# Kernel optimization log

Measured on AMD Instinct MI355X. Metric: run time of the kernel, lower is better.

## Reference

```python
import jax, jax.numpy as jnp
import numpy as np

B, C, L = 2, 512, 4096
HEADS, KV_HEADS, DIM_HEAD = 8, 2, 64
ROTARY_DIM = 32  # int(64 * 0.5), even
ROPE_THETA = 10000.0
SCALE = DIM_HEAD ** -0.5


def _rotate_half(x):
    # pairs (x0, x1) -> (-x1, x0), interleaved layout
    x = x.reshape(*x.shape[:-1], x.shape[-1] // 2, 2)
    x1, x2 = x[..., 0], x[..., 1]
    return jnp.stack([-x2, x1], axis=-1).reshape(*x.shape[:-2], x.shape[-2] * 2)


def _rope_sin_cos(seq_len, rotary_dim, theta, dtype):
    positions = jnp.arange(seq_len, dtype=dtype)
    half = rotary_dim // 2
    inv_freq = theta ** (-2.0 * jnp.arange(half, dtype=dtype) / rotary_dim)
    sinusoid = positions[:, None] * inv_freq[None, :]          # (L, half)
    sin = jnp.repeat(jnp.sin(sinusoid), 2, axis=-1)            # (L, rotary_dim) interleaved
    cos = jnp.repeat(jnp.cos(sinusoid), 2, axis=-1)
    return sin[None, None], cos[None, None]                    # (1,1,L,rotary_dim)


def setup_inputs() -> dict:
    key = jax.random.key(0)
    kx, kq, kkv, ko = jax.random.split(key, 4)
    s = 0.02
    return {
        "x": jax.random.normal(kx, (B, C, L), dtype=jnp.float32),
        "Wq": jax.random.normal(kq, (HEADS * DIM_HEAD, C), dtype=jnp.float32) * s,
        "Wkv": jax.random.normal(kkv, (2 * KV_HEADS * DIM_HEAD, C), dtype=jnp.float32) * s,
        "Wo": jax.random.normal(ko, (C, HEADS * DIM_HEAD), dtype=jnp.float32) * s,
    }


def reference(x, Wq, Wkv, Wo):
    b, c, l = x.shape
    x_t = jnp.swapaxes(x, 1, 2)                                 # (B, L, C)
    q = x_t @ Wq.T                                              # (B, L, H*dh)
    kv = x_t @ Wkv.T                                            # (B, L, KVH*2*dh)
    q = q.reshape(b, l, HEADS, DIM_HEAD).transpose(0, 2, 1, 3)  # (B, H, L, dh)
    kv = kv.reshape(b, l, KV_HEADS, 2 * DIM_HEAD).transpose(0, 2, 1, 3)
    k, v = jnp.split(kv, 2, axis=-1)                            # (B, KVH, L, dh) each

    sin, cos = _rope_sin_cos(l, ROTARY_DIM, ROPE_THETA, x.dtype)
    q_rot, q_pass = q[..., :ROTARY_DIM], q[..., ROTARY_DIM:]
    k_rot, k_pass = k[..., :ROTARY_DIM], k[..., ROTARY_DIM:]
    q_rot = q_rot * cos + _rotate_half(q_rot) * sin
    k_rot = k_rot * cos + _rotate_half(k_rot) * sin
    q = jnp.concatenate([q_rot, q_pass], axis=-1)
    k = jnp.concatenate([k_rot, k_pass], axis=-1)

    rep = HEADS // KV_HEADS
    k = jnp.repeat(k, rep, axis=1)                              # (B, H, L, dh)
    v = jnp.repeat(v, rep, axis=1)

    q = q * SCALE
    attn = jnp.einsum('bhid,bhjd->bhij', q, k)                  # (B, H, L, L)
    attn = jax.nn.softmax(attn, axis=-1)
    out = jnp.einsum('bhij,bhjd->bhid', attn, v)                # (B, H, L, dh)
    out = out.transpose(0, 2, 1, 3).reshape(b, l, HEADS * DIM_HEAD)
    out = out @ Wo.T                                            # (B, L, C)
    return jnp.swapaxes(out, 1, 2)                              # (B, C, L)
```

## Files before the change

kernel.cpp:

```cpp
#include <hip/hip_runtime.h>

using f16   = _Float16;
using f16x2 = __attribute__((ext_vector_type(2))) f16;
using f16x4 = __attribute__((ext_vector_type(4))) f16;
using f16x8 = __attribute__((ext_vector_type(8))) f16;
using f32x4 = __attribute__((ext_vector_type(4))) float;

#define L_ 4096
#define C_ 512

static __device__ __forceinline__ float fast_exp2(float x) {
#if __has_builtin(__builtin_amdgcn_exp2f)
  return __builtin_amdgcn_exp2f(x);
#else
  float r; asm("v_exp_f32 %0, %1" : "=v"(r) : "v"(x)); return r;
#endif
}

static __device__ __forceinline__ f16x2 pk2(float a, float b) {
  return __builtin_bit_cast(f16x2, __builtin_amdgcn_cvt_pkrtz(a, b));
}

#define WS_SC    0u
#define WS_WQKV  524288u
#define WS_WO    1310720u
#define WS_Q     1835008u
#define WS_K     10223616u
#define WS_VT    12320768u
#define WS_ATT   14417920u
#define WS_OP    22806528u
#define WS_LS2   56360960u
#define WS_END2  56885248u

__global__ __launch_bounds__(256) void prep_kernel(
    const float* __restrict__ Wq, const float* __restrict__ Wkv,
    const float* __restrict__ Wo,
    f16* __restrict__ wqkv, f16* __restrict__ wo16, float2* __restrict__ sc) {
  int t = blockIdx.x * 256 + threadIdx.x;
  if (t < 98304) {
    int idx = t * 4;
    float4 v = (idx < 262144) ? *(const float4*)(Wq + idx)
                              : *(const float4*)(Wkv + (idx - 262144));
    f16x4 o = {(f16)v.x, (f16)v.y, (f16)v.z, (f16)v.w};
    *(f16x4*)(wqkv + idx) = o;
  } else if (t < 163840) {
    int idx = (t - 98304) * 4;
    float4 v = *(const float4*)(Wo + idx);
    f16x4 o = {(f16)v.x, (f16)v.y, (f16)v.z, (f16)v.w};
    *(f16x4*)(wo16 + idx) = o;
  } else if (t < 229376) {
    int e = t - 163840;
    int l = e >> 4, p = e & 15;
    float invf = exp2f(-(float)p * (13.287712379549449f / 16.0f));
    float ang = (float)l * invf;
    sc[e] = make_float2(sinf(ang), cosf(ang));
  }
}

__global__ __launch_bounds__(256) void qkv_kernel(
    const float* __restrict__ x, const f16* __restrict__ wqkv,
    const float2* __restrict__ sc,
    f16* __restrict__ Qo, f16* __restrict__ Ko, f16* __restrict__ Vto) {
  int bid = blockIdx.x;
  int b   = bid / 384;
  int rem = bid % 384;
  int ot  = rem >> 7;
  int lt  = rem & 127;
  int wave = threadIdx.x >> 6, lane = threadIdx.x & 63;
  int lo = lane & 15, hi = lane >> 4;
  int obase = ot * 256 + wave * 64;
  int lbase = lt * 32;
  const float* xb = x + (size_t)b * C_ * L_;

  f32x4 acc[4][2] = {};
  for (int kc = 0; kc < 512; kc += 32) {
    f16x8 aw[4];
#pragma unroll
    for (int oc = 0; oc < 4; ++oc)
      aw[oc] = *(const f16x8*)(wqkv + (obase + oc * 16 + lo) * 512 + kc + hi * 8);
#pragma unroll
    for (int lc = 0; lc < 2; ++lc) {
      f16x8 bx;
#pragma unroll
      for (int i = 0; i < 8; ++i)
        bx[i] = (f16)xb[(size_t)(kc + hi * 8 + i) * L_ + lbase + lc * 16 + lo];
#pragma unroll
      for (int oc = 0; oc < 4; ++oc)
        acc[oc][lc] = __builtin_amdgcn_mfma_f32_16x16x32_f16(aw[oc], bx, acc[oc][lc], 0, 0, 0);
    }
  }

  bool is_q = obase < 512;
  int  og   = obase - 512;
  int  kvh  = is_q ? 0 : (og >> 7);
  bool is_v = (!is_q) && ((og & 127) == 64);
  int  h    = obase >> 6;
  const float QSCALE = 0.125f * 1.44269504088896340736f;

#pragma unroll
  for (int oc = 0; oc < 4; ++oc) {
#pragma unroll
    for (int lc = 0; lc < 2; ++lc) {
      f32x4 v = acc[oc][lc];
      int l = lbase + lc * 16 + lo;
      int d = oc * 16 + hi * 4;
      if (!is_v && oc < 2) {
        int p0 = d >> 1;
        float2 s0 = sc[l * 16 + p0];
        float2 s1 = sc[l * 16 + p0 + 1];
        float a0 = v[0], a1 = v[1], a2 = v[2], a3 = v[3];
        v[0] = a0 * s0.y - a1 * s0.x;
        v[1] = a1 * s0.y + a0 * s0.x;
        v[2] = a2 * s1.y - a3 * s1.x;
        v[3] = a3 * s1.y + a2 * s1.x;
      }
      if (is_q) {
        f16x4 st = {(f16)(v[0] * QSCALE), (f16)(v[1] * QSCALE),
                    (f16)(v[2] * QSCALE), (f16)(v[3] * QSCALE)};
        *(f16x4*)(Qo + (((size_t)b * 8 + h) * L_ + l) * 64 + d) = st;
      } else if (!is_v) {
        f16x4 st = {(f16)v[0], (f16)v[1], (f16)v[2], (f16)v[3]};
        *(f16x4*)(Ko + (((size_t)b * 2 + kvh) * L_ + l) * 64 + d) = st;
      } else {
#pragma unroll
        for (int i = 0; i < 4; ++i)
          Vto[(((size_t)b * 2 + kvh) * 64 + d + i) * L_ + l] = (f16)v[i];
      }
    }
  }
}

template <int SPLIT>
__global__ __launch_bounds__(512) void attn_kernel(
    const f16* __restrict__ Qi, const f16* __restrict__ Ki,
    const f16* __restrict__ Vti, f16* __restrict__ att,
    f16* __restrict__ opart, float* __restrict__ lsews) {
  __shared__ __align__(16) char smem[2][16384];
  int bid  = blockIdx.x;
  int half = (SPLIT > 1) ? (bid >> 7) : 0;
  int rem7 = bid & 127;
  int b   = rem7 >> 6;
  int rr  = rem7 & 63;
  int h   = rr >> 3;
  int qt  = rr & 7;
  int tid  = threadIdx.x;
  int wave = tid >> 6, lane = tid & 63;
  int lo = lane & 15, hi = lane >> 4;
  int kvh = h >> 2;
  const f16*  Qp   = Qi + ((size_t)(b * 8 + h) * L_) * 64;
  const char* Ksrc = (const char*)(Ki  + ((size_t)(b * 2 + kvh)) * L_ * 64)
                     + (size_t)half * (L_ / SPLIT) * 128;
  const char* Vsrc = (const char*)(Vti + ((size_t)(b * 2 + kvh)) * 64 * L_)
                     + (size_t)half * (L_ / SPLIT) * 2;

  int lqb = qt * 512 + wave * 64;
  f16x8 qf[4][2];
#pragma unroll
  for (int qi = 0; qi < 4; ++qi)
#pragma unroll
    for (int hf = 0; hf < 2; ++hf)
      qf[qi][hf] = *(const f16x8*)(Qp + (size_t)(lqb + qi * 16 + lo) * 64 + hf * 32 + hi * 8);

  int c0 = tid;
  int r0 = c0 >> 3, m0 = c0 & 7;
  int cb0 = m0 << 4;
  int dstK0 = r0 * 128 + (cb0 ^ ((r0 & 7) << 4));
  int ca0 = (m0 >> 2) * 64 + ((2 * m0) & 3) * 16 + ((m0 >> 1) & 1) * 8;
  int dstV0a = r0 * 128 + (ca0 ^ ((r0 & 7) << 4));
  int dstV0b = r0 * 128 + ((ca0 + 16) ^ ((r0 & 7) << 4));

  f16x8 sK0, sV0;
#define STAGE_LOAD(t) do {                                            \
    sK0 = *(const f16x8*)(Ksrc + (size_t)(t) * 8192 + c0 * 16);       \
    sV0 = *(const f16x8*)(Vsrc + (size_t)r0 * 8192 + (t) * 128 + cb0);\
  } while (0)
#define STAGE_WRITE(base_) do {                                       \
    char* kb_ = (char*)(base_);                                       \
    *(f16x8*)(kb_ + dstK0) = sK0;                                     \
    *(f16x4*)(kb_ + 8192 + dstV0a) = __builtin_shufflevector(sV0, sV0, 0, 1, 2, 3); \
    *(f16x4*)(kb_ + 8192 + dstV0b) = __builtin_shufflevector(sV0, sV0, 4, 5, 6, 7); \
  } while (0)

  f32x4 oacc[4][4] = {};
  f32x4 lse[4] = {};
  const f16x8 ones8 = {(f16)1.f, (f16)1.f, (f16)1.f, (f16)1.f,
                       (f16)1.f, (f16)1.f, (f16)1.f, (f16)1.f};
  int swz = (lo & 7) << 4;

#define COMPUTE(buf_) do {                                                          \
    const char* kb = (const char*)(buf_);                                           \
    const char* vb = kb + 8192;                                                     \
    _Pragma("unroll")                                                               \
    for (int jp = 0; jp < 2; ++jp) {                                                \
      f32x4 s[2][4] = {};                                                           \
      __builtin_amdgcn_s_setprio(1);                                                \
      _Pragma("unroll")                                                             \
      for (int jj = 0; jj < 2; ++jj) {                                              \
        int j = jp * 2 + jj;                                                        \
        f16x8 ka0 = *(const f16x8*)(kb + (j * 16 + lo) * 128 + ((hi * 16) ^ swz));  \
        f16x8 ka1 = *(const f16x8*)(kb + (j * 16 + lo) * 128 + ((64 + hi * 16) ^ swz)); \
        _Pragma("unroll")                                                           \
        for (int qi = 0; qi < 4; ++qi) {                                            \
          s[jj][qi] = __builtin_amdgcn_mfma_f32_16x16x32_f16(ka0, qf[qi][0], s[jj][qi], 0, 0, 0); \
          s[jj][qi] = __builtin_amdgcn_mfma_f32_16x16x32_f16(ka1, qf[qi][1], s[jj][qi], 0, 0, 0); \
        }                                                                           \
      }                                                                             \
      __builtin_amdgcn_s_setprio(0);                                                \
      f16x8 pc[4];                                                                  \
      _Pragma("unroll")                                                             \
      for (int qi = 0; qi < 4; ++qi) {                                              \
        f16x2 a0 = pk2(fast_exp2(s[0][qi][0]), fast_exp2(s[0][qi][1]));             \
        f16x2 a1 = pk2(fast_exp2(s[0][qi][2]), fast_exp2(s[0][qi][3]));             \
        f16x2 b0 = pk2(fast_exp2(s[1][qi][0]), fast_exp2(s[1][qi][1]));             \
        f16x2 b1 = pk2(fast_exp2(s[1][qi][2]), fast_exp2(s[1][qi][3]));             \
        f16x4 l4 = __builtin_shufflevector(a0, a1, 0, 1, 2, 3);                     \
        f16x4 h4 = __builtin_shufflevector(b0, b1, 0, 1, 2, 3);                     \
        pc[qi] = __builtin_shufflevector(l4, h4, 0, 1, 2, 3, 4, 5, 6, 7);           \
      }                                                                             \
      __builtin_amdgcn_s_setprio(1);                                                \
      _Pragma("unroll")                                                             \
      for (int dc = 0; dc < 4; ++dc) {                                              \
        f16x8 vv = *(const f16x8*)(vb + (dc * 16 + lo) * 128 + ((jp * 64 + hi * 16) ^ swz)); \
        _Pragma("unroll")                                                           \
        for (int qi = 0; qi < 4; ++qi)                                              \
          oacc[dc][qi] = __builtin_amdgcn_mfma_f32_16x16x32_f16(vv, pc[qi], oacc[dc][qi], 0, 0, 0); \
      }                                                                             \
      _Pragma("unroll")                                                             \
      for (int qi = 0; qi < 4; ++qi)                                                \
        lse[qi] = __builtin_amdgcn_mfma_f32_16x16x32_f16(ones8, pc[qi], lse[qi], 0, 0, 0); \
      __builtin_amdgcn_s_setprio(0);                                                \
    }                                                                               \
  } while (0)

  const int NT = 64 / SPLIT;
  STAGE_LOAD(0);
  STAGE_WRITE(smem[0]);
  __syncthreads();

  for (int t = 0; t < NT; t += 2) {
    STAGE_LOAD(t + 1);
    COMPUTE(smem[0]);
    STAGE_WRITE(smem[1]);
    __syncthreads();
    if (t + 2 < NT) STAGE_LOAD(t + 2);
    COMPUTE(smem[1]);
    if (t + 2 < NT) STAGE_WRITE(smem[0]);
    __syncthreads();
  }

#pragma unroll
  for (int qi = 0; qi < 4; ++qi) {
    int lq = lqb + qi * 16 + lo;
    if constexpr (SPLIT > 1) {
      size_t obase = (((size_t)(half * 2 + b) * 8 + h) * L_ + lq) * 64;
#pragma unroll
      for (int dc = 0; dc < 4; ++dc) {
        f16x4 st;
#pragma unroll
        for (int i = 0; i < 4; ++i) st[i] = (f16)oacc[dc][qi][i];
        *(f16x4*)(opart + obase + dc * 16 + hi * 4) = st;
      }
      if (hi == 0)
        lsews[((size_t)(half * 2 + b) * 8 + h) * L_ + lq] = lse[qi][0];
    } else {
      float inv = 1.f / lse[qi][0];
#pragma unroll
      for (int dc = 0; dc < 4; ++dc) {
        f16x4 st;
#pragma unroll
        for (int i = 0; i < 4; ++i) st[i] = (f16)(oacc[dc][qi][i] * inv);
        *(f16x4*)(att + ((size_t)b * L_ + lq) * 512 + h * 64 + dc * 16 + hi * 4) = st;
      }
    }
  }
#undef STAGE_LOAD
#undef STAGE_WRITE
#undef COMPUTE
}

template <int SPLIT>
__global__ __launch_bounds__(256) void combine_kernel(
    const f16* __restrict__ opart, const float* __restrict__ lsews,
    f16* __restrict__ att) {
  int t = blockIdx.x * 256 + threadIdx.x;
  int d4 = t & 15;
  int lq = (t >> 4) & 4095;
  int h  = (t >> 16) & 7;
  int b  = t >> 19;
  const size_t HS  = (size_t)2 * 8 * 4096 * 64;
  const size_t LSS = (size_t)2 * 8 * 4096;
  size_t base  = (((size_t)b * 8 + h) * 4096 + lq) * 64 + d4 * 4;
  size_t lbase = ((size_t)b * 8 + h) * 4096 + lq;
  float o[4] = {};
  float ls = 0.f;
#pragma unroll
  for (int s = 0; s < SPLIT; ++s) {
    f16x4 op = *(const f16x4*)(opart + s * HS + base);
#pragma unroll
    for (int i = 0; i < 4; ++i) o[i] += (float)op[i];
    ls += lsews[s * LSS + lbase];
  }
  float inv = 1.f / ls;
  f16x4 st;
#pragma unroll
  for (int i = 0; i < 4; ++i) st[i] = (f16)(o[i] * inv);
  *(f16x4*)(att + ((size_t)b * 4096 + lq) * 512 + h * 64 + d4 * 4) = st;
}

__global__ __launch_bounds__(256) void oproj_kernel(
    const f16* __restrict__ att, const f16* __restrict__ wo16,
    float* __restrict__ out) {
  int bid = blockIdx.x;
  int b   = bid / 256;
  int rem = bid % 256;
  int ct  = rem >> 7;
  int lt  = rem & 127;
  int wave = threadIdx.x >> 6, lane = threadIdx.x & 63;
  int lo = lane & 15, hi = lane >> 4;
  int cobase = ct * 256 + wave * 64;
  int lbase  = lt * 32;
  const f16* ab = att + (size_t)b * L_ * 512;

  f32x4 acc[4][2] = {};
  for (int kc = 0; kc < 512; kc += 32) {
    f16x8 aw[4];
#pragma unroll
    for (int cc = 0; cc < 4; ++cc)
      aw[cc] = *(const f16x8*)(wo16 + (cobase + cc * 16 + lo) * 512 + kc + hi * 8);
#pragma unroll
    for (int lc = 0; lc < 2; ++lc) {
      f16x8 bx = *(const f16x8*)(ab + (size_t)(lbase + lc * 16 + lo) * 512 + kc + hi * 8);
#pragma unroll
      for (int cc = 0; cc < 4; ++cc)
        acc[cc][lc] = __builtin_amdgcn_mfma_f32_16x16x32_f16(aw[cc], bx, acc[cc][lc], 0, 0, 0);
    }
  }
  float* ob = out + (size_t)b * C_ * L_;
#pragma unroll
  for (int cc = 0; cc < 4; ++cc)
#pragma unroll
    for (int lc = 0; lc < 2; ++lc) {
      int l = lbase + lc * 16 + lo;
#pragma unroll
      for (int i = 0; i < 4; ++i) {
        int co = cobase + cc * 16 + hi * 4 + i;
        ob[(size_t)co * L_ + l] = acc[cc][lc][i];
      }
    }
}

extern "C" void kernel_launch(void* const* d_in, const int* in_sizes, int n_in,
                              void* d_out, int out_size, void* d_ws, size_t ws_size,
                              hipStream_t stream) {
  const float* x   = (const float*)d_in[0];
  const float* Wq  = (const float*)d_in[1];
  const float* Wkv = (const float*)d_in[2];
  const float* Wo  = (const float*)d_in[3];
  char* ws = (char*)d_ws;
  float2* sc  = (float2*)(ws + WS_SC);
  f16* wqkv   = (f16*)(ws + WS_WQKV);
  f16* wo16   = (f16*)(ws + WS_WO);
  f16* Qb     = (f16*)(ws + WS_Q);
  f16* Kb     = (f16*)(ws + WS_K);
  f16* Vtb    = (f16*)(ws + WS_VT);
  f16* attb   = (f16*)(ws + WS_ATT);
  f16* opb    = (f16*)(ws + WS_OP);
  float* lsb  = (float*)(ws + WS_LS2);

  prep_kernel<<<1024, 256, 0, stream>>>(Wq, Wkv, Wo, wqkv, wo16, sc);
  qkv_kernel<<<768, 256, 0, stream>>>(x, wqkv, sc, Qb, Kb, Vtb);
  if (ws_size >= (size_t)WS_END2) {
    attn_kernel<2><<<256, 512, 0, stream>>>(Qb, Kb, Vtb, attb, opb, lsb);
    combine_kernel<2><<<4096, 256, 0, stream>>>(opb, lsb, attb);
  } else {
    attn_kernel<1><<<128, 512, 0, stream>>>(Qb, Kb, Vtb, attb, opb, lsb);
  }
  oproj_kernel<<<512, 256, 0, stream>>>(attb, wo16, (float*)d_out);
}
```

Measured before the change: 144.5 us.

## Fuse split-KV combine into output projection and halve attention block size

The attention kernel now launches 256-thread blocks covering 256 query rows each, with each thread staging two K/V chunks per tile. The launch doubles the grid to 512 blocks for better CU coverage and occupancy. The separate combine kernel is removed. The output projection reads both partial outputs and their log-sum-exp sums directly, normalizes them while building the MFMA B operand, and so avoids writing and re-reading the intermediate attention buffer. In exchange, the projection does redundant combine work per column tile (two ct tiles) and reads partials with strided 64-element accesses.

```diff
diff --git a/kernel.cpp b/kernel.cpp
--- a/kernel.cpp
+++ b/kernel.cpp
@@ -131,18 +131,18 @@
 }
 
 template <int SPLIT>
-__global__ __launch_bounds__(512) void attn_kernel(
+__global__ __launch_bounds__(256) void attn_kernel(
     const f16* __restrict__ Qi, const f16* __restrict__ Ki,
     const f16* __restrict__ Vti, f16* __restrict__ att,
     f16* __restrict__ opart, float* __restrict__ lsews) {
   __shared__ __align__(16) char smem[2][16384];
   int bid  = blockIdx.x;
-  int half = (SPLIT > 1) ? (bid >> 7) : 0;
-  int rem7 = bid & 127;
-  int b   = rem7 >> 6;
-  int rr  = rem7 & 63;
-  int h   = rr >> 3;
-  int qt  = rr & 7;
+  int half = (SPLIT > 1) ? (bid >> 8) : 0;
+  int rem8 = bid & 255;
+  int b   = rem8 >> 7;
+  int rr  = rem8 & 127;
+  int h   = rr >> 4;
+  int qt  = rr & 15;
   int tid  = threadIdx.x;
   int wave = tid >> 6, lane = tid & 63;
   int lo = lane & 15, hi = lane >> 4;
@@ -153,7 +153,7 @@
   const char* Vsrc = (const char*)(Vti + ((size_t)(b * 2 + kvh)) * 64 * L_)
                      + (size_t)half * (L_ / SPLIT) * 2;
 
-  int lqb = qt * 512 + wave * 64;
+  int lqb = qt * 256 + wave * 64;
   f16x8 qf[4][2];
 #pragma unroll
   for (int qi = 0; qi < 4; ++qi)
@@ -161,24 +161,34 @@
     for (int hf = 0; hf < 2; ++hf)
       qf[qi][hf] = *(const f16x8*)(Qp + (size_t)(lqb + qi * 16 + lo) * 64 + hf * 32 + hi * 8);
 
-  int c0 = tid;
+  int c0 = tid, c1 = tid + 256;
   int r0 = c0 >> 3, m0 = c0 & 7;
-  int cb0 = m0 << 4;
+  int r1 = c1 >> 3, m1 = c1 & 7;
+  int cb0 = m0 << 4, cb1 = m1 << 4;
   int dstK0 = r0 * 128 + (cb0 ^ ((r0 & 7) << 4));
+  int dstK1 = r1 * 128 + (cb1 ^ ((r1 & 7) << 4));
   int ca0 = (m0 >> 2) * 64 + ((2 * m0) & 3) * 16 + ((m0 >> 1) & 1) * 8;
+  int ca1 = (m1 >> 2) * 64 + ((2 * m1) & 3) * 16 + ((m1 >> 1) & 1) * 8;
   int dstV0a = r0 * 128 + (ca0 ^ ((r0 & 7) << 4));
   int dstV0b = r0 * 128 + ((ca0 + 16) ^ ((r0 & 7) << 4));
-
-  f16x8 sK0, sV0;
+  int dstV1a = r1 * 128 + (ca1 ^ ((r1 & 7) << 4));
+  int dstV1b = r1 * 128 + ((ca1 + 16) ^ ((r1 & 7) << 4));
+
+  f16x8 sK0, sK1, sV0, sV1;
 #define STAGE_LOAD(t) do {                                            \
     sK0 = *(const f16x8*)(Ksrc + (size_t)(t) * 8192 + c0 * 16);       \
+    sK1 = *(const f16x8*)(Ksrc + (size_t)(t) * 8192 + c1 * 16);       \
     sV0 = *(const f16x8*)(Vsrc + (size_t)r0 * 8192 + (t) * 128 + cb0);\
+    sV1 = *(const f16x8*)(Vsrc + (size_t)r1 * 8192 + (t) * 128 + cb1);\
   } while (0)
 #define STAGE_WRITE(base_) do {                                       \
     char* kb_ = (char*)(base_);                                       \
     *(f16x8*)(kb_ + dstK0) = sK0;                                     \
+    *(f16x8*)(kb_ + dstK1) = sK1;                                     \
     *(f16x4*)(kb_ + 8192 + dstV0a) = __builtin_shufflevector(sV0, sV0, 0, 1, 2, 3); \
     *(f16x4*)(kb_ + 8192 + dstV0b) = __builtin_shufflevector(sV0, sV0, 4, 5, 6, 7); \
+    *(f16x4*)(kb_ + 8192 + dstV1a) = __builtin_shufflevector(sV1, sV1, 0, 1, 2, 3); \
+    *(f16x4*)(kb_ + 8192 + dstV1b) = __builtin_shufflevector(sV1, sV1, 4, 5, 6, 7); \
   } while (0)
 
   f32x4 oacc[4][4] = {};
@@ -278,33 +288,68 @@
 #undef COMPUTE
 }
 
-template <int SPLIT>
-__global__ __launch_bounds__(256) void combine_kernel(
+__global__ __launch_bounds__(256) void oproj_fused_kernel(
     const f16* __restrict__ opart, const float* __restrict__ lsews,
-    f16* __restrict__ att) {
-  int t = blockIdx.x * 256 + threadIdx.x;
-  int d4 = t & 15;
-  int lq = (t >> 4) & 4095;
-  int h  = (t >> 16) & 7;
-  int b  = t >> 19;
+    const f16* __restrict__ wo16, float* __restrict__ out) {
+  int bid = blockIdx.x;
+  int b   = bid / 256;
+  int rem = bid % 256;
+  int ct  = rem >> 7;
+  int lt  = rem & 127;
+  int wave = threadIdx.x >> 6, lane = threadIdx.x & 63;
+  int lo = lane & 15, hi = lane >> 4;
+  int cobase = ct * 256 + wave * 64;
+  int lbase  = lt * 32;
   const size_t HS  = (size_t)2 * 8 * 4096 * 64;
   const size_t LSS = (size_t)2 * 8 * 4096;
-  size_t base  = (((size_t)b * 8 + h) * 4096 + lq) * 64 + d4 * 4;
-  size_t lbase = ((size_t)b * 8 + h) * 4096 + lq;
-  float o[4] = {};
-  float ls = 0.f;
-#pragma unroll
-  for (int s = 0; s < SPLIT; ++s) {
-    f16x4 op = *(const f16x4*)(opart + s * HS + base);
-#pragma unroll
-    for (int i = 0; i < 4; ++i) o[i] += (float)op[i];
-    ls += lsews[s * LSS + lbase];
-  }
-  float inv = 1.f / ls;
-  f16x4 st;
-#pragma unroll
-  for (int i = 0; i < 4; ++i) st[i] = (f16)(o[i] * inv);
-  *(f16x4*)(att + ((size_t)b * 4096 + lq) * 512 + h * 64 + d4 * 4) = st;
+
+  float inv[2][8];
+#pragma unroll
+  for (int lc = 0; lc < 2; ++lc) {
+    int l = lbase + lc * 16 + lo;
+#pragma unroll
+    for (int h = 0; h < 8; ++h) {
+      size_t lidx = ((size_t)b * 8 + h) * L_ + l;
+      inv[lc][h] = 1.f / (lsews[lidx] + lsews[LSS + lidx]);
+    }
+  }
+
+  f32x4 acc[4][2] = {};
+  for (int kc = 0; kc < 512; kc += 32) {
+    f16x8 aw[4];
+#pragma unroll
+    for (int cc = 0; cc < 4; ++cc)
+      aw[cc] = *(const f16x8*)(wo16 + (cobase + cc * 16 + lo) * 512 + kc + hi * 8);
+#pragma unroll
+    for (int lc = 0; lc < 2; ++lc) {
+      int l = lbase + lc * 16 + lo;
+      int o = kc + hi * 8;
+      int h = o >> 6, d = o & 63;
+      size_t base = (((size_t)b * 8 + h) * L_ + l) * 64 + d;
+      f16x8 p0 = *(const f16x8*)(opart + base);
+      f16x8 p1 = *(const f16x8*)(opart + HS + base);
+      float iv = inv[lc][h];
+      f16x8 bx;
+#pragma unroll
+      for (int i = 0; i < 8; ++i)
+        bx[i] = (f16)(((float)p0[i] + (float)p1[i]) * iv);
+#pragma unroll
+      for (int cc = 0; cc < 4; ++cc)
+        acc[cc][lc] = __builtin_amdgcn_mfma_f32_16x16x32_f16(aw[cc], bx, acc[cc][lc], 0, 0, 0);
+    }
+  }
+  float* ob = out + (size_t)b * C_ * L_;
+#pragma unroll
+  for (int cc = 0; cc < 4; ++cc)
+#pragma unroll
+    for (int lc = 0; lc < 2; ++lc) {
+      int l = lbase + lc * 16 + lo;
+#pragma unroll
+      for (int i = 0; i < 4; ++i) {
+        int co = cobase + cc * 16 + hi * 4 + i;
+        ob[(size_t)co * L_ + l] = acc[cc][lc][i];
+      }
+    }
 }
 
 __global__ __launch_bounds__(256) void oproj_kernel(
@@ -370,10 +415,10 @@
   prep_kernel<<<1024, 256, 0, stream>>>(Wq, Wkv, Wo, wqkv, wo16, sc);
   qkv_kernel<<<768, 256, 0, stream>>>(x, wqkv, sc, Qb, Kb, Vtb);
   if (ws_size >= (size_t)WS_END2) {
-    attn_kernel<2><<<256, 512, 0, stream>>>(Qb, Kb, Vtb, attb, opb, lsb);
-    combine_kernel<2><<<4096, 256, 0, stream>>>(opb, lsb, attb);
+    attn_kernel<2><<<512, 256, 0, stream>>>(Qb, Kb, Vtb, attb, opb, lsb);
+    oproj_fused_kernel<<<512, 256, 0, stream>>>(opb, lsb, wo16, (float*)d_out);
   } else {
-    attn_kernel<1><<<128, 512, 0, stream>>>(Qb, Kb, Vtb, attb, opb, lsb);
-  }
-  oproj_kernel<<<512, 256, 0, stream>>>(attb, wo16, (float*)d_out);
-}
+    attn_kernel<1><<<256, 256, 0, stream>>>(Qb, Kb, Vtb, attb, opb, lsb);
+    oproj_kernel<<<512, 256, 0, stream>>>(attb, wo16, (float*)d_out);
+  }
+}
```

Measured after the change: 158.0 us. 9.3% more time.

## Pre-swizzle K/V tiles in projection and load them straight into LDS

Applied to the files above, without the earlier changes.

The projection kernel now writes K and V to global memory already tiled and XOR-swizzled in exactly the shared-memory layout the attention kernel uses. The attention kernel can then copy each tile with 16-byte global_load_lds transfers directly into LDS, skipping the round trip through registers and the separate LDS writes. The double-buffered loop becomes one stage per iteration with a single barrier. In exchange, the layouts of the two kernels are now tightly coupled, and correctness relies on the barrier waiting for the async LDS loads to finish.

```diff
diff --git a/kernel.cpp b/kernel.cpp
--- a/kernel.cpp
+++ b/kernel.cpp
@@ -19,6 +19,12 @@
 
 static __device__ __forceinline__ f16x2 pk2(float a, float b) {
   return __builtin_bit_cast(f16x2, __builtin_amdgcn_cvt_pkrtz(a, b));
+}
+
+static __device__ __forceinline__ void gl16(const char* g, char* l) {
+  __builtin_amdgcn_global_load_lds(
+      (const __attribute__((address_space(1))) unsigned int*)g,
+      (__attribute__((address_space(3))) unsigned int*)l, 16, 0, 0);
 }
 
 #define WS_SC    0u
@@ -120,11 +126,22 @@
         *(f16x4*)(Qo + (((size_t)b * 8 + h) * L_ + l) * 64 + d) = st;
       } else if (!is_v) {
         f16x4 st = {(f16)v[0], (f16)v[1], (f16)v[2], (f16)v[3]};
-        *(f16x4*)(Ko + (((size_t)b * 2 + kvh) * L_ + l) * 64 + d) = st;
+        int t = l >> 6, r = l & 63;
+        int u = (d >> 3) ^ (r & 7);
+        int w = (hi & 1) * 8;
+        char* Kb = (char*)Ko + (size_t)(b * 2 + kvh) * (L_ * 128);
+        *(f16x4*)(Kb + (size_t)t * 8192 + r * 128 + u * 16 + w) = st;
       } else {
-#pragma unroll
-        for (int i = 0; i < 4; ++i)
-          Vto[(((size_t)b * 2 + kvh) * 64 + d + i) * L_ + l] = (f16)v[i];
+        int t = l >> 6, kk = l & 63;
+        int m = kk >> 3, i8 = kk & 7;
+        int ca = (m >> 2) * 64 + ((2 * m) & 3) * 16 + ((m >> 1) & 1) * 8;
+        int bcol = ca + (i8 < 4 ? 2 * i8 : 8 + 2 * i8);
+        char* Vb = (char*)Vto + (size_t)(b * 2 + kvh) * (L_ * 128);
+#pragma unroll
+        for (int i = 0; i < 4; ++i) {
+          int rv = d + i;
+          *(f16*)(Vb + (size_t)t * 8192 + rv * 128 + (bcol ^ ((rv & 7) << 4))) = (f16)v[i];
+        }
       }
     }
   }
@@ -148,10 +165,10 @@
   int lo = lane & 15, hi = lane >> 4;
   int kvh = h >> 2;
   const f16*  Qp   = Qi + ((size_t)(b * 8 + h) * L_) * 64;
-  const char* Ksrc = (const char*)(Ki  + ((size_t)(b * 2 + kvh)) * L_ * 64)
+  const char* Ksrc = (const char*)Ki  + (size_t)(b * 2 + kvh) * (L_ * 128)
                      + (size_t)half * (L_ / SPLIT) * 128;
-  const char* Vsrc = (const char*)(Vti + ((size_t)(b * 2 + kvh)) * 64 * L_)
-                     + (size_t)half * (L_ / SPLIT) * 2;
+  const char* Vsrc = (const char*)Vti + (size_t)(b * 2 + kvh) * (L_ * 128)
+                     + (size_t)half * (L_ / SPLIT) * 128;
 
   int lqb = qt * 512 + wave * 64;
   f16x8 qf[4][2];
@@ -162,23 +179,9 @@
       qf[qi][hf] = *(const f16x8*)(Qp + (size_t)(lqb + qi * 16 + lo) * 64 + hf * 32 + hi * 8);
 
   int c0 = tid;
-  int r0 = c0 >> 3, m0 = c0 & 7;
-  int cb0 = m0 << 4;
-  int dstK0 = r0 * 128 + (cb0 ^ ((r0 & 7) << 4));
-  int ca0 = (m0 >> 2) * 64 + ((2 * m0) & 3) * 16 + ((m0 >> 1) & 1) * 8;
-  int dstV0a = r0 * 128 + (ca0 ^ ((r0 & 7) << 4));
-  int dstV0b = r0 * 128 + ((ca0 + 16) ^ ((r0 & 7) << 4));
-
-  f16x8 sK0, sV0;
-#define STAGE_LOAD(t) do {                                            \
-    sK0 = *(const f16x8*)(Ksrc + (size_t)(t) * 8192 + c0 * 16);       \
-    sV0 = *(const f16x8*)(Vsrc + (size_t)r0 * 8192 + (t) * 128 + cb0);\
-  } while (0)
-#define STAGE_WRITE(base_) do {                                       \
-    char* kb_ = (char*)(base_);                                       \
-    *(f16x8*)(kb_ + dstK0) = sK0;                                     \
-    *(f16x4*)(kb_ + 8192 + dstV0a) = __builtin_shufflevector(sV0, sV0, 0, 1, 2, 3); \
-    *(f16x4*)(kb_ + 8192 + dstV0b) = __builtin_shufflevector(sV0, sV0, 4, 5, 6, 7); \
+#define STAGE(t, base_) do {                                           \
+    gl16(Ksrc + (size_t)(t) * 8192 + c0 * 16, (char*)(base_) + c0 * 16); \
+    gl16(Vsrc + (size_t)(t) * 8192 + c0 * 16, (char*)(base_) + 8192 + c0 * 16); \
   } while (0)
 
   f32x4 oacc[4][4] = {};
@@ -233,18 +236,12 @@
   } while (0)
 
   const int NT = 64 / SPLIT;
-  STAGE_LOAD(0);
-  STAGE_WRITE(smem[0]);
+  STAGE(0, smem[0]);
   __syncthreads();
 
-  for (int t = 0; t < NT; t += 2) {
-    STAGE_LOAD(t + 1);
-    COMPUTE(smem[0]);
-    STAGE_WRITE(smem[1]);
-    __syncthreads();
-    if (t + 2 < NT) STAGE_LOAD(t + 2);
-    COMPUTE(smem[1]);
-    if (t + 2 < NT) STAGE_WRITE(smem[0]);
+  for (int t = 0; t < NT; ++t) {
+    if (t + 1 < NT) STAGE(t + 1, smem[(t + 1) & 1]);
+    COMPUTE(smem[t & 1]);
     __syncthreads();
   }
 
@@ -273,8 +270,7 @@
       }
     }
   }
-#undef STAGE_LOAD
-#undef STAGE_WRITE
+#undef STAGE
 #undef COMPUTE
 }
 
```

After: 145.2 us. About the same (+0.4%).
